# Kernel tuning notes

Hardware: AMD Instinct MI355X
Metric: run time of the kernel (lower is better)

## Reference

```python
import jax, jax.numpy as jnp
import numpy as np

C = 256
RED = 8
D = C // RED  # qk dim = 32
EPS = 1e-5   # nn.LayerNorm default


def setup_inputs() -> dict:
    key = jax.random.key(0)
    ks = jax.random.split(key, 10)
    B, H, W = 4, 64, 64
    s = 0.02
    return {
        "x": jax.random.normal(ks[0], (B, C, H, W), dtype=jnp.float32),
        "wq": jax.random.normal(ks[1], (D, C), dtype=jnp.float32) * s,
        "bq": jax.random.normal(ks[2], (D,), dtype=jnp.float32) * s,
        "wk": jax.random.normal(ks[3], (D, C), dtype=jnp.float32) * s,
        "bk": jax.random.normal(ks[4], (D,), dtype=jnp.float32) * s,
        "wv": jax.random.normal(ks[5], (C, C), dtype=jnp.float32) * s,
        "bv": jax.random.normal(ks[6], (C,), dtype=jnp.float32) * s,
        "gamma": jax.random.normal(ks[7], (1,), dtype=jnp.float32) * 0.1,
        "ln_w": jnp.ones((C,), dtype=jnp.float32),
        "ln_b": jnp.zeros((C,), dtype=jnp.float32),
    }


def reference(x, wq, bq, wk, bk, wv, bv, gamma, ln_w, ln_b):
    B, Cc, H, W = x.shape
    N = H * W
    xf = x.reshape(B, Cc, N)  # [B,C,N]
    # 1x1 convs == per-pixel linear over channels
    q = jnp.einsum('dc,bcn->bnd', wq, xf) + bq              # [B,N,D]
    k = jnp.einsum('dc,bcn->bdn', wk, xf) + bk[:, None]     # [B,D,N]
    v = jnp.einsum('ec,bcn->ben', wv, xf) + bv[:, None]     # [B,C,N]
    scale = 1.0 / (D ** 0.5)
    scores = jnp.einsum('bnd,bdm->bnm', q, k) * scale       # [B,N,N]
    # original subtracts row max then softmax; jax.nn.softmax is equivalent & stable
    attn = jax.nn.softmax(scores, axis=-1)                  # [B,N,N]
    out = jnp.einsum('bcm,bnm->bcn', v, attn)               # [B,C,N]
    res = gamma[0] * out + xf                               # gamma residual
    # LayerNorm over channel dim (module permutes to channels-last)
    r = res.transpose(0, 2, 1)                              # [B,N,C]
    mu = jnp.mean(r, axis=-1, keepdims=True)
    var = jnp.mean(jnp.square(r - mu), axis=-1, keepdims=True)
    y = (r - mu) * jax.lax.rsqrt(var + EPS) * ln_w + ln_b
    return y.transpose(0, 2, 1).reshape(B, Cc, H, W)
```

## Files before the change

kernel.cpp:

```cpp
#include <hip/hip_runtime.h>
#include <hip/hip_bf16.h>

#define NPIX 4096
#define NCH  256

typedef __attribute__((ext_vector_type(8))) short short8;
typedef __attribute__((ext_vector_type(16))) float f32x16;
typedef __attribute__((ext_vector_type(2))) unsigned int u32x2;
typedef __attribute__((ext_vector_type(8))) int i32x8;

union Frag64 { long l[4]; i32x8 v; };

#define SC1 0x7F7F7F7F

__device__ inline unsigned short bfbits(float f) {
    __hip_bfloat16 h = __float2bfloat16(f);
    return *reinterpret_cast<unsigned short*>(&h);
}

__device__ inline unsigned int pkfp8x4(float a, float b, float c, float d) {
    int w = __builtin_amdgcn_cvt_pk_fp8_f32(a, b, 0, false);
    w = __builtin_amdgcn_cvt_pk_fp8_f32(c, d, w, true);
    return (unsigned int)w;
}

__device__ inline unsigned char fp8b(float a) {
    return (unsigned char)(__builtin_amdgcn_cvt_pk_fp8_f32(a, a, 0, false) & 0xff);
}

__device__ inline float bperm(int srclane, float v) {
    return __int_as_float(__builtin_amdgcn_ds_bpermute(
        srclane << 2, __float_as_int(v)));
}

__global__ void __launch_bounds__(256) prep_kernel(
    const float* __restrict__ x,
    const float* __restrict__ wq, const float* __restrict__ bq,
    const float* __restrict__ wk, const float* __restrict__ bk,
    const float* __restrict__ wv, const float* __restrict__ bv,
    __hip_bfloat16* __restrict__ Wc, float* __restrict__ bc,
    __hip_bfloat16* __restrict__ XTg)
{
    const int bid = blockIdx.x;
    const int t   = threadIdx.x;
    if (bid >= 1024) {
        const int j = bid - 1024;
        const float kQ = 0.17677669529663687f * 1.4426950408889634f;
        const float* src;
        float sc = 1.0f;
        if (j < 32)       { src = wq + j * 256; }
        else if (j < 64)  { src = wk + (j - 32) * 256; sc = kQ; }
        else              { src = wv + (j - 64) * 256; }
        Wc[j * 256 + t] = __float2bfloat16(src[t] * sc);
        if (t == 0) {
            float bb = (j < 32) ? bq[j] : (j < 64) ? bk[j - 32] * kQ : bv[j - 64];
            bc[j] = bb;
        }
        return;
    }
    __shared__ float xs[64][65];
    const int b  = bid >> 8;
    const int c0 = ((bid >> 6) & 3) * 64;
    const int n0 = (bid & 63) * 64;
    const float* xb = x + ((size_t)b * NCH + c0) * NPIX + n0;
    #pragma unroll 4
    for (int i = 0; i < 16; ++i) {
        int c = i * 4 + (t >> 6);
        int n = t & 63;
        xs[c][n] = xb[(size_t)c * NPIX + n];
    }
    __syncthreads();
    #pragma unroll 4
    for (int i = 0; i < 16; ++i) {
        int nn = i * 4 + (t >> 6);
        int cL = t & 63;
        XTg[((size_t)b * NPIX + n0 + nn) * NCH + c0 + cL] =
            __float2bfloat16(xs[cL][nn]);
    }
}

__global__ void __launch_bounds__(256) proj_kernel(
    const __hip_bfloat16* __restrict__ Wc, const float* __restrict__ bc,
    const __hip_bfloat16* __restrict__ XTg,
    unsigned char* __restrict__ Q8, unsigned char* __restrict__ K8,
    unsigned char* __restrict__ V8)
{
    const int b    = blockIdx.z;
    const int t    = threadIdx.x;
    const int lane = t & 63;
    const int wid  = t >> 6;
    const int lo   = lane & 31;
    const int hi   = lane >> 5;
    const int n0   = blockIdx.x * 128 + wid * 32;

    short8 xf[16];
    const __hip_bfloat16* xr = XTg + ((size_t)b * NPIX + n0 + lo) * NCH;
    #pragma unroll
    for (int ks = 0; ks < 16; ++ks)
        xf[ks] = *(const short8*)(xr + ks * 16 + hi * 8);

    for (int jt = 0; jt < 10; ++jt) {
        f32x16 acc;
        #pragma unroll
        for (int r = 0; r < 16; ++r) acc[r] = 0.f;
        const __hip_bfloat16* wr = Wc + (size_t)(jt * 32 + lo) * NCH;
        #pragma unroll
        for (int ks = 0; ks < 16; ++ks) {
            short8 wf = *(const short8*)(wr + ks * 16 + hi * 8);
            acc = __builtin_amdgcn_mfma_f32_32x32x16_bf16(wf, xf[ks], acc, 0, 0, 0);
        }
        if (jt < 2) {
            unsigned char* dst = (jt == 0 ? Q8 : K8)
                               + ((size_t)b * NPIX + n0 + lo) * 32;
            #pragma unroll
            for (int g = 0; g < 4; ++g) {
                int jr = 8 * g + 4 * hi;
                unsigned int w = pkfp8x4(acc[4 * g + 0] + bc[jt * 32 + jr + 0],
                                         acc[4 * g + 1] + bc[jt * 32 + jr + 1],
                                         acc[4 * g + 2] + bc[jt * 32 + jr + 2],
                                         acc[4 * g + 3] + bc[jt * 32 + jr + 3]);
                *(unsigned int*)(dst + jr) = w;
            }
        } else {
            unsigned char* vb = V8 + (size_t)b * NPIX * NCH
                              + (size_t)((n0 + lo) >> 4) * 4096 + (lo & 15);
            #pragma unroll
            for (int r = 0; r < 16; ++r) {
                int jr = (r & 3) + 8 * (r >> 2) + 4 * hi;
                int c  = jt * 32 + jr - 64;
                vb[(size_t)c * 16] = fp8b(acc[r] + bc[jt * 32 + jr]);
            }
        }
    }
}

__global__ void __launch_bounds__(512, 4) attn_kernel(
    const unsigned char* __restrict__ Q8, const unsigned char* __restrict__ K8,
    const unsigned char* __restrict__ V8, const __hip_bfloat16* __restrict__ XTg,
    const float* __restrict__ gamma_p, const float* __restrict__ lnw,
    const float* __restrict__ lnb, float* __restrict__ out)
{
    __shared__ char smem[39936];

    const int t    = threadIdx.x;
    const int lane = t & 63;
    const int wid  = t >> 6;
    const int lo   = lane & 31;
    const int hi   = lane >> 5;

    const int lid = blockIdx.y * 128 + blockIdx.x;
    const int xcd = lid & 7;
    const int b   = xcd >> 1;
    const int q0  = ((xcd & 1) * 64 + (lid >> 3)) * 32;

    const unsigned char* Qb = Q8 + ((size_t)b * NPIX + q0) * 32;
    Frag64 qv;
    qv.l[0] = *(const long*)(Qb + lo * 32 + hi * 8);
    qv.l[1] = *(const long*)(Qb + lo * 32 + 16 + hi * 8);
    qv.l[2] = 0; qv.l[3] = 0;

    const unsigned char* Kw = K8 + (size_t)b * NPIX * 32
                            + (size_t)(wid * 32 + lo) * 32 + hi * 8;
    const unsigned char* Vw = V8 + (size_t)b * NPIX * NCH
                            + (size_t)(32 * wid + lo) * 16 + hi * 8;

    f32x16 acc;
    #pragma unroll
    for (int r = 0; r < 16; ++r) acc[r] = 0.f;
    f32x16 z16;
    #pragma unroll
    for (int r = 0; r < 16; ++r) z16[r] = 0.f;
    float s_run = 0.f;

    long kA0 = *(const long*)(Kw);
    long kA1 = *(const long*)(Kw + 16);
    long kB0 = kA0, kB1 = kA1;

    const int swz = lo & 15;

    for (int it = 0; it < 16; ++it) {
        long vv[16];
        const unsigned char* vit = Vw + (size_t)(it * 16) * 4096;
        #pragma unroll
        for (int s = 0; s < 16; ++s)
            vv[s] = *(const long*)(vit + (size_t)s * 4096);

        if (it < 15) {
            kB0 = *(const long*)(Kw + (size_t)(it + 1) * 8192);
            kB1 = *(const long*)(Kw + (size_t)(it + 1) * 8192 + 16);
        }

        Frag64 ka;
        ka.l[0] = kA0; ka.l[1] = kA1; ka.l[2] = 0; ka.l[3] = 0;
        f32x16 sct = __builtin_amdgcn_mfma_scale_f32_32x32x64_f8f6f4(
            ka.v, qv.v, z16, 0, 0, 0, SC1, 0, SC1);

        char* pb = smem + (it & 1) * 8192 + lo * 256 + 4 * hi;
        float psum = 0.f;
        #pragma unroll
        for (int g = 0; g < 4; ++g) {
            float e0 = __builtin_exp2f(sct[4 * g + 0]);
            float e1 = __builtin_exp2f(sct[4 * g + 1]);
            float e2 = __builtin_exp2f(sct[4 * g + 2]);
            float e3 = __builtin_exp2f(sct[4 * g + 3]);
            psum += (e0 + e1) + (e2 + e3);
            unsigned int w = pkfp8x4(e0, e1, e2, e3);
            int gran = (4 * wid + g) ^ swz;
            *(unsigned int*)(pb + gran * 8) = w;
        }
        psum += __shfl_xor(psum, 32);
        s_run += psum;

        __syncthreads();

        const char* pr = smem + (it & 1) * 8192 + lo * 256;
        __builtin_amdgcn_s_setprio(1);
        #pragma unroll
        for (int s = 0; s < 4; ++s) {
            Frag64 pa, vb;
            #pragma unroll
            for (int p = 0; p < 4; ++p) {
                int gran = (8 * s + 2 * p + hi) ^ swz;
                pa.l[p] = *(const long*)(pr + gran * 8);
                vb.l[p] = vv[4 * s + p];
            }
            acc = __builtin_amdgcn_mfma_scale_f32_32x32x64_f8f6f4(
                pa.v, vb.v, acc, 0, 0, 0, SC1, 0, SC1);
        }
        __builtin_amdgcn_s_setprio(0);
        kA0 = kB0; kA1 = kB1;
    }

    float* red_sp = (float*)(smem + 36864);
    float* red2p  = (float*)(smem + 37888);
    float (*ybuf)[36] = (float(*)[36])smem;

    if (hi == 0) red_sp[wid * 32 + lo] = s_run;
    __syncthreads();
    float stot = 0.f;
    #pragma unroll
    for (int w = 0; w < 8; ++w) stot += red_sp[w * 32 + lo];
    const float invs = 1.0f / stot;
    const float gamma = gamma_p[0];
    const int cL = 32 * wid + lo;
    const __hip_bfloat16* XTb = XTg + ((size_t)b * NPIX + q0) * NCH + cL;
    float rv[16];
    #pragma unroll
    for (int r = 0; r < 16; ++r) {
        int qr = (r & 3) + 8 * (r >> 2) + 4 * hi;
        float ir = bperm(qr, invs);
        float xv = __bfloat162float(XTb[(size_t)qr * NCH]);
        rv[r] = gamma * (acc[r] * ir) + xv;
        float s1 = rv[r];
        float s2 = rv[r] * rv[r];
        #pragma unroll
        for (int off = 1; off < 32; off <<= 1) {
            s1 += __shfl_xor(s1, off);
            s2 += __shfl_xor(s2, off);
        }
        if (lo == 0) {
            red2p[qr * 16 + wid * 2]     = s1;
            red2p[qr * 16 + wid * 2 + 1] = s2;
        }
    }
    __syncthreads();
    float sA = 0.f, sB = 0.f;
    #pragma unroll
    for (int w = 0; w < 8; ++w) {
        sA += red2p[lo * 16 + w * 2];
        sB += red2p[lo * 16 + w * 2 + 1];
    }
    const float mean = sA * (1.f / 256.f);
    const float var  = sB * (1.f / 256.f) - mean * mean;
    const float rstd = rsqrtf(var + 1e-5f);
    const float lwv = lnw[cL];
    const float lbv = lnb[cL];
    #pragma unroll
    for (int r = 0; r < 16; ++r) {
        int qr = (r & 3) + 8 * (r >> 2) + 4 * hi;
        float m  = bperm(qr, mean);
        float rr = bperm(qr, rstd);
        ybuf[cL][qr] = (rv[r] - m) * rr * lwv + lbv;
    }
    __syncthreads();
    const int c_r = t >> 1;
    const int qh  = (t & 1) * 16;
    float* dst = out + ((size_t)b * NCH + c_r) * NPIX + q0 + qh;
    #pragma unroll
    for (int j = 0; j < 4; ++j) {
        float4 v;
        v.x = ybuf[c_r][qh + j * 4 + 0];
        v.y = ybuf[c_r][qh + j * 4 + 1];
        v.z = ybuf[c_r][qh + j * 4 + 2];
        v.w = ybuf[c_r][qh + j * 4 + 3];
        *(float4*)(dst + j * 4) = v;
    }
}

extern "C" void kernel_launch(void* const* d_in, const int* in_sizes, int n_in,
                              void* d_out, int out_size, void* d_ws, size_t ws_size,
                              hipStream_t stream) {
    const float* x     = (const float*)d_in[0];
    const float* wq    = (const float*)d_in[1];
    const float* bq    = (const float*)d_in[2];
    const float* wk    = (const float*)d_in[3];
    const float* bk    = (const float*)d_in[4];
    const float* wv    = (const float*)d_in[5];
    const float* bv    = (const float*)d_in[6];
    const float* gamma = (const float*)d_in[7];
    const float* ln_w  = (const float*)d_in[8];
    const float* ln_b  = (const float*)d_in[9];
    float* out = (float*)d_out;

    const int B = 4;
    unsigned char* ws = (unsigned char*)d_ws;
    unsigned char*  Q8 = ws;
    unsigned char*  K8 = ws + (512u << 10);
    unsigned char*  V8 = ws + (1u << 20);
    __hip_bfloat16* XT = (__hip_bfloat16*)(ws + (5u << 20));
    __hip_bfloat16* Wc = (__hip_bfloat16*)(ws + (13u << 20));
    float*          bc = (float*)(ws + (13u << 20) + 163840);

    prep_kernel<<<dim3(1344), 256, 0, stream>>>(x, wq, bq, wk, bk, wv, bv,
                                                Wc, bc, XT);
    proj_kernel<<<dim3(32, 1, B), 256, 0, stream>>>(Wc, bc, XT, Q8, K8, V8);
    attn_kernel<<<dim3(128, B), 512, 0, stream>>>(Q8, K8, V8, XT, gamma,
                                                  ln_w, ln_b, out);
}
```

Baseline: 104.2 us.

## Software-pipeline attention loop and split projection output tiles across two blocks

The attention loop is restructured so the P·V MFMAs for the previous tile run before the exp/softmax of the current tile. The V loads for the next tile are issued during that work, which overlaps global loads with compute and shortens the dependency chain ahead of each barrier. Separately, the projection kernel splits its ten output tiles across two blocks in the y dimension, doubling the grid to improve occupancy at the cost of reloading the X fragments. The prologue and epilogue peel the first and last iterations, which adds code size and register pressure from the held V fragments.

```diff
diff --git a/kernel.cpp b/kernel.cpp
--- a/kernel.cpp
+++ b/kernel.cpp
@@ -92,6 +92,7 @@
     const int lo   = lane & 31;
     const int hi   = lane >> 5;
     const int n0   = blockIdx.x * 128 + wid * 32;
+    const int jb   = blockIdx.y * 5;
 
     short8 xf[16];
     const __hip_bfloat16* xr = XTg + ((size_t)b * NPIX + n0 + lo) * NCH;
@@ -99,7 +100,8 @@
     for (int ks = 0; ks < 16; ++ks)
         xf[ks] = *(const short8*)(xr + ks * 16 + hi * 8);
 
-    for (int jt = 0; jt < 10; ++jt) {
+    for (int jo = 0; jo < 5; ++jo) {
+        const int jt = jb + jo;
         f32x16 acc;
         #pragma unroll
         for (int r = 0; r < 16; ++r) acc[r] = 0.f;
@@ -172,30 +174,27 @@
     for (int r = 0; r < 16; ++r) z16[r] = 0.f;
     float s_run = 0.f;
 
-    long kA0 = *(const long*)(Kw);
-    long kA1 = *(const long*)(Kw + 16);
-    long kB0 = kA0, kB1 = kA1;
-
     const int swz = lo & 15;
 
-    for (int it = 0; it < 16; ++it) {
-        long vv[16];
-        const unsigned char* vit = Vw + (size_t)(it * 16) * 4096;
-        #pragma unroll
-        for (int s = 0; s < 16; ++s)
-            vv[s] = *(const long*)(vit + (size_t)s * 4096);
-
-        if (it < 15) {
-            kB0 = *(const long*)(Kw + (size_t)(it + 1) * 8192);
-            kB1 = *(const long*)(Kw + (size_t)(it + 1) * 8192 + 16);
-        }
-
-        Frag64 ka;
-        ka.l[0] = kA0; ka.l[1] = kA1; ka.l[2] = 0; ka.l[3] = 0;
+    Frag64 ka;
+    ka.l[0] = *(const long*)(Kw);
+    ka.l[1] = *(const long*)(Kw + 16);
+    ka.l[2] = 0; ka.l[3] = 0;
+    long kB0 = 0, kB1 = 0;
+
+    Frag64 vva[4];
+    #pragma unroll
+    for (int s = 0; s < 4; ++s)
+        #pragma unroll
+        for (int p = 0; p < 4; ++p)
+            vva[s].l[p] = *(const long*)(Vw + (size_t)(4 * s + p) * 4096);
+
+    {
         f32x16 sct = __builtin_amdgcn_mfma_scale_f32_32x32x64_f8f6f4(
             ka.v, qv.v, z16, 0, 0, 0, SC1, 0, SC1);
-
-        char* pb = smem + (it & 1) * 8192 + lo * 256 + 4 * hi;
+        kB0 = *(const long*)(Kw + 8192);
+        kB1 = *(const long*)(Kw + 8192 + 16);
+        char* pb = smem + lo * 256 + 4 * hi;
         float psum = 0.f;
         #pragma unroll
         for (int g = 0; g < 4; ++g) {
@@ -210,25 +209,75 @@
         }
         psum += __shfl_xor(psum, 32);
         s_run += psum;
-
-        __syncthreads();
-
-        const char* pr = smem + (it & 1) * 8192 + lo * 256;
+    }
+    __syncthreads();
+
+    for (int it = 1; it < 16; ++it) {
+        ka.l[0] = kB0; ka.l[1] = kB1;
+        f32x16 sct = __builtin_amdgcn_mfma_scale_f32_32x32x64_f8f6f4(
+            ka.v, qv.v, z16, 0, 0, 0, SC1, 0, SC1);
+
+        const char* pr = smem + ((it - 1) & 1) * 8192 + lo * 256;
         __builtin_amdgcn_s_setprio(1);
         #pragma unroll
         for (int s = 0; s < 4; ++s) {
-            Frag64 pa, vb;
+            Frag64 pa;
             #pragma unroll
             for (int p = 0; p < 4; ++p) {
                 int gran = (8 * s + 2 * p + hi) ^ swz;
                 pa.l[p] = *(const long*)(pr + gran * 8);
-                vb.l[p] = vv[4 * s + p];
             }
             acc = __builtin_amdgcn_mfma_scale_f32_32x32x64_f8f6f4(
-                pa.v, vb.v, acc, 0, 0, 0, SC1, 0, SC1);
+                pa.v, vva[s].v, acc, 0, 0, 0, SC1, 0, SC1);
         }
         __builtin_amdgcn_s_setprio(0);
-        kA0 = kB0; kA1 = kB1;
+
+        if (it < 15) {
+            kB0 = *(const long*)(Kw + (size_t)(it + 1) * 8192);
+            kB1 = *(const long*)(Kw + (size_t)(it + 1) * 8192 + 16);
+        }
+
+        const unsigned char* vit = Vw + (size_t)it * 65536;
+        #pragma unroll
+        for (int s = 0; s < 4; ++s)
+            #pragma unroll
+            for (int p = 0; p < 4; ++p)
+                vva[s].l[p] = *(const long*)(vit + (size_t)(4 * s + p) * 4096);
+
+        char* pb = smem + (it & 1) * 8192 + lo * 256 + 4 * hi;
+        float psum = 0.f;
+        #pragma unroll
+        for (int g = 0; g < 4; ++g) {
+            float e0 = __builtin_exp2f(sct[4 * g + 0]);
+            float e1 = __builtin_exp2f(sct[4 * g + 1]);
+            float e2 = __builtin_exp2f(sct[4 * g + 2]);
+            float e3 = __builtin_exp2f(sct[4 * g + 3]);
+            psum += (e0 + e1) + (e2 + e3);
+            unsigned int w = pkfp8x4(e0, e1, e2, e3);
+            int gran = (4 * wid + g) ^ swz;
+            *(unsigned int*)(pb + gran * 8) = w;
+        }
+        psum += __shfl_xor(psum, 32);
+        s_run += psum;
+
+        __syncthreads();
+    }
+
+    {
+        const char* pr = smem + 8192 + lo * 256;
+        __builtin_amdgcn_s_setprio(1);
+        #pragma unroll
+        for (int s = 0; s < 4; ++s) {
+            Frag64 pa;
+            #pragma unroll
+            for (int p = 0; p < 4; ++p) {
+                int gran = (8 * s + 2 * p + hi) ^ swz;
+                pa.l[p] = *(const long*)(pr + gran * 8);
+            }
+            acc = __builtin_amdgcn_mfma_scale_f32_32x32x64_f8f6f4(
+                pa.v, vva[s].v, acc, 0, 0, 0, SC1, 0, SC1);
+        }
+        __builtin_amdgcn_s_setprio(0);
     }
 
     float* red_sp = (float*)(smem + 36864);
@@ -323,7 +372,7 @@
 
     prep_kernel<<<dim3(1344), 256, 0, stream>>>(x, wq, bq, wk, bk, wv, bv,
                                                 Wc, bc, XT);
-    proj_kernel<<<dim3(32, 1, B), 256, 0, stream>>>(Wc, bc, XT, Q8, K8, V8);
+    proj_kernel<<<dim3(32, 2, B), 256, 0, stream>>>(Wc, bc, XT, Q8, K8, V8);
     attn_kernel<<<dim3(128, B), 512, 0, stream>>>(Q8, K8, V8, XT, gamma,
                                                   ln_w, ln_b, out);
 }
```

Result: faster. 87.89 us (-15.6%).
